# Kernel optimization log

Measured on AMD Instinct MI355X. Metric: run time of the kernel, lower is better.

Reference implementation:

```python
import jax, jax.numpy as jnp
import numpy as np

B, L, NV = 16, 512, 321
D, PL, ST = 128, 16, 8
P = (L - PL) // ST + 2  # 64 patches (replication pad of `stride` on the right)
E, K, H = 8, 2, 512     # experts, top-n gates, expert hidden (4*d_model)
PRED = 96
BAL_COEF, Z_COEF = 0.01, 0.001


def sinusoidal_pe(n, d):
    pos = np.arange(n)[:, None].astype(np.float32)
    div = np.exp(np.arange(0, d, 2).astype(np.float32) * -(np.log(10000.0) / d))
    pe = np.zeros((n, d), dtype=np.float32)
    pe[:, 0::2] = np.sin(pos * div)
    pe[:, 1::2] = np.cos(pos * div)
    return jnp.asarray(pe)


def setup_inputs() -> dict:
    key = jax.random.key(0)
    ks = jax.random.split(key, 12)
    s = lambda i, shape, sc: jax.random.normal(ks[i], shape, jnp.float32) * sc
    return {
        "x_enc": jax.random.normal(ks[0], (B, L, NV), jnp.float32),
        "x_mark_enc": jax.random.normal(ks[1], (B, L, 4), jnp.float32),
        "x_dec": jax.random.normal(ks[2], (B, PRED, NV), jnp.float32),
        "x_mark_dec": jax.random.normal(ks[3], (B, PRED, 4), jnp.float32),
        "W_val": s(4, (PL, D), PL ** -0.5),
        "W_g": s(5, (D, E), D ** -0.5),
        "W1": s(6, (E, D, H), D ** -0.5),
        "b1": jnp.zeros((E, H), jnp.float32),
        "W2": s(7, (E, H, D), H ** -0.5),
        "b2": jnp.zeros((E, D), jnp.float32),
        "W_head": s(8, (D * P, PRED), (D * P) ** -0.5),
        "b_head": jnp.zeros((PRED,), jnp.float32),
    }


def _forward(x_enc, W_val, W_g, W1, b1, W2, b2, W_head, b_head):
    # RevIN-style instance norm (means detached as in torch .detach())
    means = jax.lax.stop_gradient(jnp.mean(x_enc, axis=1, keepdims=True))
    xc = x_enc - means
    stdev = jnp.sqrt(jnp.var(xc, axis=1, keepdims=True) + 1e-5)
    xn = xc / stdev

    # Patch embedding: [B, NV, L] -> replicate-pad -> unfold -> linear + sinusoidal PE
    x = jnp.transpose(xn, (0, 2, 1))                        # [B, NV, L]
    x = jnp.pad(x, ((0, 0), (0, 0), (0, ST)), mode="edge")  # ReplicationPad1d((0, stride))
    idx = np.arange(P)[:, None] * ST + np.arange(PL)        # [P, PL]
    patches = x[:, :, idx]                                  # [B, NV, P, PL]
    tok = patches.reshape(B * NV, P, PL)
    emb = tok @ W_val + sinusoidal_pe(P, D)[None]           # [N, P, D]

    # MoE: top-n softmax gating (gates not renormalized), balance + router-z aux losses
    t = emb.reshape(-1, D)                                  # [T, D], T = B*NV*P
    logits = t @ W_g                                        # [T, E]
    probs = jax.nn.softmax(logits, axis=-1)
    topv, topi = jax.lax.top_k(probs, K)                    # [T, K]

    out = jnp.zeros_like(t)
    for e in range(E):  # fixed small expert count; each expert is a GELU MLP
        h = jax.nn.gelu(t @ W1[e] + b1[e], approximate=False) @ W2[e] + b2[e]
        g = jnp.sum(jnp.where(topi == e, topv, 0.0), axis=-1)  # gate for expert e (0 if unrouted)
        out = out + g[:, None] * h

    me = jnp.mean(probs, axis=0)                                            # mean router prob per expert
    ce = jnp.mean(jax.nn.one_hot(topi, E, dtype=probs.dtype).sum(1), 0) / K  # dispatch fraction per expert
    balance_loss = E * jnp.sum(me * ce)
    z_loss = jnp.mean(jax.nn.logsumexp(logits, axis=-1) ** 2)
    aux = BAL_COEF * balance_loss + Z_COEF * z_loss

    # FlattenHead: [B, NV, P, D] -> [B, NV, D, P] -> flatten(-2) -> Linear(nf, pred_len)
    enc = out.reshape(B, NV, P, D).transpose(0, 1, 3, 2)    # [B, NV, D, P]
    dec = enc.reshape(B, NV, D * P) @ W_head + b_head        # [B, NV, PRED]
    dec = jnp.transpose(dec, (0, 2, 1))                      # [B, PRED, NV]

    # de-normalize
    dec = dec * stdev[:, 0][:, None, :] + means[:, 0][:, None, :]
    return dec, aux


def reference(x_enc, x_mark_enc, x_dec, x_mark_dec, W_val, W_g, W1, b1, W2, b2, W_head, b_head):
    return _forward(x_enc, W_val, W_g, W1, b1, W2, b2, W_head, b_head)
```

## Files before the change

### kernel.cpp

```cpp
#include <hip/hip_runtime.h>
#include <hip/hip_bf16.h>

typedef unsigned short u16;
typedef unsigned int   u32;
typedef unsigned long long u64;
typedef __attribute__((ext_vector_type(8))) short bf16x8;
typedef __attribute__((ext_vector_type(4))) float f32x4;
typedef __attribute__((ext_vector_type(16))) float f32x16;

#define MFMA16(a,b,c) __builtin_amdgcn_mfma_f32_16x16x32_bf16(a,b,c,0,0,0)
#define MFMA32(a,b,c) __builtin_amdgcn_mfma_f32_32x32x16_bf16(a,b,c,0,0,0)

#define NV_   321
#define B_    16
#define L_    512
#define D_    128
#define P_    64
#define E_    8
#define H_    512
#define NRW   5136
#define NTOK  328704
#define DP_   8192
#define NBUCK 329728

static __device__ __forceinline__ u16 f2bf(float f){
  __hip_bfloat16 h = __float2bfloat16(f);
  return *reinterpret_cast<u16*>(&h);
}

static __device__ __forceinline__ float gelu_f(float x){
  float x2 = x*x;
  float p  = __builtin_fmaf(-0.1029433f, x2, -2.3022083f);
  float a  = x*p;
  float en = exp2f(a);
  float r  = __builtin_amdgcn_rcpf(1.0f + en);
  return x*r;
}

static __device__ __forceinline__ u32 bfadd2(u32 a, u32 b){
  float lo = __uint_as_float(a<<16)           + __uint_as_float(b<<16);
  float hi = __uint_as_float(a&0xffff0000u)   + __uint_as_float(b&0xffff0000u);
  return (u32)f2bf(lo) | ((u32)f2bf(hi)<<16);
}

static constexpr size_t alup(size_t x){ return (x + 255) & ~(size_t)255; }
static constexpr size_t OFF_MEAN = 0;
static constexpr size_t OFF_RSTD = OFF_MEAN + alup((size_t)NRW*4);
static constexpr size_t OFF_STD  = OFF_RSTD + alup((size_t)NRW*4);
static constexpr size_t OFF_XT   = OFF_STD  + alup((size_t)NRW*4);
static constexpr size_t OFF_PE   = OFF_XT   + alup((size_t)NRW*L_*4);
static constexpr size_t OFF_W1T  = OFF_PE   + alup((size_t)P_*D_*4);
static constexpr size_t OFF_W2T  = OFF_W1T  + alup((size_t)E_*H_*D_*2);
static constexpr size_t OFF_WHT  = OFF_W2T  + alup((size_t)E_*D_*H_*2);
static constexpr size_t OFF_T    = OFF_WHT  + alup((size_t)96*DP_*2);
static constexpr size_t OFF_TOPI = OFF_T    + alup((size_t)NTOK*D_*2);
static constexpr size_t OFF_GATE = OFF_TOPI + alup((size_t)NTOK*4);
static constexpr size_t OFF_CNTR = OFF_GATE + alup((size_t)NTOK*8);
static constexpr size_t OFF_BTOK = OFF_CNTR + alup((size_t)1024);
static constexpr size_t OFF_BGT  = OFF_BTOK + alup((size_t)2*NBUCK*4);
static constexpr size_t OFF_OUT  = OFF_BGT  + alup((size_t)2*NBUCK*4);
static constexpr size_t OFF_MEAND= OFF_OUT  + alup((size_t)NTOK*D_*2);
static constexpr size_t OFF_RSTDD= OFF_MEAND+ alup((size_t)NRW*8);
static constexpr size_t OFF_WVG  = OFF_RSTDD+ alup((size_t)NRW*8);
static constexpr size_t OFF_PEG  = OFF_WVG  + alup((size_t)16*8*8);
static constexpr size_t OFF_PG   = OFF_PEG  + alup((size_t)P_*E_*8);
static constexpr size_t OFF_PI   = OFF_PG   + alup((size_t)NRW*12*4);



__global__ void k_xt(const float* __restrict__ x, float* __restrict__ xT){
  __shared__ float tile[32][33];
  int b = blockIdx.z;
  int v0 = blockIdx.x*32, l0 = blockIdx.y*32;
  int tx = threadIdx.x, ty = threadIdx.y;
  for(int i=ty;i<32;i+=8){
    int l = l0+i, v = v0+tx;
    tile[i][tx] = (v<NV_) ? x[((size_t)b*L_ + l)*NV_ + v] : 0.f;
  }
  __syncthreads();
  for(int i=ty;i<32;i+=8){
    int v = v0+i, l = l0+tx;
    if(v<NV_) xT[((size_t)(b*NV_+v))*L_ + l] = tile[tx][i];
  }
}

__global__ void k_stats(const float* __restrict__ xT, float* meanp, float* rstdp, float* stdp,
                        double* meand, double* rstdd){
  __shared__ double s1[256], s2[256];
  int r = blockIdx.x, t = threadIdx.x;
  double a = (double)xT[(size_t)r*L_ + t], b = (double)xT[(size_t)r*L_ + 256 + t];
  s1[t]=a+b; s2[t]=a*a+b*b;
  __syncthreads();
  for(int o=128;o>0;o>>=1){ if(t<o){ s1[t]+=s1[t+o]; s2[t]+=s2[t+o]; } __syncthreads(); }
  if(t==0){
    double m = s1[0]*(1.0/512.0);
    double var = s2[0]*(1.0/512.0) - m*m;
    double sd = sqrt(var + 1e-5);
    meanp[r]=(float)m; stdp[r]=(float)sd; rstdp[r]=(float)(1.0/sd);
    meand[r]=m; rstdd[r]=1.0/sd;
  }
}

__global__ void k_prep(const float* __restrict__ Wval, const float* __restrict__ Wg,
                       float* __restrict__ pef, double* __restrict__ Wvg,
                       double* __restrict__ peg){
  int t = threadIdx.x;
  for(int i=t;i<8192;i+=256){
    int p = i>>7, d = i&127, k = d>>1;
    double div = exp(-(double)(2*k) * (9.210340371976184 /128.0));
    double ang = (double)p * div;
    double v = (d&1) ? cos(ang) : sin(ang);
    pef[i] = (float)v;
  }
  __syncthreads();
  if(t<128){
    int j = t>>3, e = t&7;
    double acc = 0.0;
    for(int d=0;d<128;d++) acc += (double)Wval[j*128+d] * (double)Wg[d*8+e];
    Wvg[t] = acc;
  }
  for(int q=t;q<512;q+=256){
    int p = q>>3, e = q&7;
    double acc = 0.0;
    for(int d=0;d<128;d++) acc += (double)pef[p*128+d] * (double)Wg[d*8+e];
    peg[q] = acc;
  }
}

__global__ void k_wt(const float* __restrict__ in, u16* __restrict__ outp, int R, int C){
  __shared__ float tile[32][33];
  int e = blockIdx.z;
  int c0 = blockIdx.x*32, r0 = blockIdx.y*32;
  const float* src = in + (size_t)e*R*C;
  u16* dst = outp + (size_t)e*R*C;
  int tx=threadIdx.x, ty=threadIdx.y;
  for(int i=ty;i<32;i+=8){
    int r=r0+i, c=c0+tx;
    tile[i][tx] = (r<R && c<C) ? src[(size_t)r*C+c] : 0.f;
  }
  __syncthreads();
  for(int i=ty;i<32;i+=8){
    int c=c0+i, r=r0+tx;
    if(c<C && r<R) dst[(size_t)c*R + r] = f2bf(tile[tx][i]);
  }
}

__global__ void k_wh(const float* __restrict__ Wh, u16* __restrict__ WhT2){
  __shared__ float tile[32][33];
  int d0 = blockIdx.x*32, o0 = blockIdx.y*32, p = blockIdx.z;
  int tx = threadIdx.x, ty = threadIdx.y;
  for(int i=ty;i<32;i+=8){
    int r = (d0+i)*64 + p;
    tile[i][tx] = Wh[(size_t)r*96 + o0 + tx];
  }
  __syncthreads();
  for(int i=ty;i<32;i+=8){
    int o = o0+i;
    WhT2[(size_t)o*DP_ + p*128 + d0 + tx] = f2bf(tile[tx][i]);
  }
}

__global__ __launch_bounds__(256) void k_embed(
    const float* __restrict__ xT, const float* __restrict__ meanp, const float* __restrict__ rstdp,
    const float* __restrict__ Wval, const float* __restrict__ pe,
    u16* __restrict__ tglob)
{
  __shared__ __align__(16) float xn[520];
  int r = blockIdx.x, t = threadIdx.x;
  float mean = meanp[r], rstd = rstdp[r];
  float v0 = (xT[(size_t)r*L_ + t]       - mean)*rstd;
  float v1 = (xT[(size_t)r*L_ + 256 + t] - mean)*rstd;
  xn[t] = v0; xn[t+256] = v1;
  if(t==255){
    #pragma unroll
    for(int i=512;i<520;i++) xn[i]=v1;
  }
  int d0 = (t & 63)*2;
  int p0 = t >> 6;
  float2 w[16];
  #pragma unroll
  for(int j=0;j<16;j++) w[j] = *(const float2*)(Wval + j*128 + d0);
  __syncthreads();

  for(int p=p0;p<64;p+=4){
    const float4* xp = (const float4*)(xn + p*8);
    float4 x0=xp[0], x1=xp[1], x2=xp[2], x3=xp[3];
    float xv[16];
    *(float4*)(xv+0)=x0; *(float4*)(xv+4)=x1; *(float4*)(xv+8)=x2; *(float4*)(xv+12)=x3;
    float2 pw = *(const float2*)(pe + p*128 + d0);
    float a0 = pw.x, a1 = pw.y;
    #pragma unroll
    for(int j=0;j<16;j++){ a0 += xv[j]*w[j].x; a1 += xv[j]*w[j].y; }
    u32 packed = (u32)f2bf(a0) | ((u32)f2bf(a1)<<16);
    *(u32*)(tglob + ((size_t)(r*64+p)*128 + d0)) = packed;
  }
}

__global__ __launch_bounds__(256) void k_gate(
    const float* __restrict__ xT, const double* __restrict__ meand, const double* __restrict__ rstdd,
    const double* __restrict__ Wvg, const double* __restrict__ peg,
    int* __restrict__ topip, float2* __restrict__ gatep,
    float* __restrict__ pg, int* __restrict__ pib)
{
  __shared__ double xn[520];
  __shared__ double lgt[64][9];
  int r = blockIdx.x, t = threadIdx.x;
  double m = meand[r], rs = rstdd[r];
  double v0 = ((double)xT[(size_t)r*L_ + t]       - m)*rs;
  double v1 = ((double)xT[(size_t)r*L_ + 256 + t] - m)*rs;
  xn[t]=v0; xn[t+256]=v1;
  if(t==255){
    #pragma unroll
    for(int i=512;i<520;i++) xn[i]=v1;
  }
  __syncthreads();
  for(int q=t;q<512;q+=256){
    int p = q>>3, e = q&7;
    double acc = peg[q];
    #pragma unroll
    for(int j=0;j<16;j++) acc += xn[p*8+j]*Wvg[j*8+e];
    lgt[p][e] = acc;
  }
  __syncthreads();
  if(t<64){
    int token = r*64 + t;
    double l0[8];
    #pragma unroll
    for(int e=0;e<8;e++) l0[e]=lgt[t][e];
    double mx=l0[0];
    #pragma unroll
    for(int e=1;e<8;e++) mx = fmax(mx,l0[e]);
    int i1=0; double b1v=l0[0];
    #pragma unroll
    for(int e=1;e<8;e++) if(l0[e]>b1v){b1v=l0[e]; i1=e;}
    int i2=-1; double b2v=-1e300;
    #pragma unroll
    for(int e=0;e<8;e++) if(e!=i1 && l0[e]>b2v){b2v=l0[e]; i2=e;}
    float pr[8]; float sum=0.f;
    #pragma unroll
    for(int e=0;e<8;e++){ pr[e]=__expf((float)(l0[e]-mx)); sum+=pr[e]; }
    float inv = 1.f/sum;
    #pragma unroll
    for(int e=0;e<8;e++) pr[e]*=inv;
    topip[token] = i1 | (i2<<8);
    gatep[token] = make_float2(pr[i1], pr[i2]);
    float lse = (float)mx + __logf(sum);
    #pragma unroll
    for(int e=0;e<8;e++){
      float v = pr[e];
      for(int o=32;o>0;o>>=1) v += __shfl_down(v,o);
      if(t==0) pg[r*12+e] = v;
    }
    {
      float z = lse*lse;
      for(int o=32;o>0;o>>=1) z += __shfl_down(z,o);
      if(t==0) pg[r*12+8] = z;
    }
    #pragma unroll
    for(int e=0;e<8;e++){
      u64 m1 = __ballot(i1==e);
      u64 m2 = __ballot(i2==e);
      if(t==0){
        pib[r*16+e]   = (int)__popcll(m1);
        pib[r*16+8+e] = (int)__popcll(m2);
      }
    }
  }
}

__global__ __launch_bounds__(256) void k_aux(const float* __restrict__ pg, const int* __restrict__ pib,
                                             int* __restrict__ ci, float* __restrict__ dout){
  __shared__ double sd[256];
  __shared__ int si[256];
  __shared__ double totd[9];
  __shared__ int toti[16];
  int t = threadIdx.x;
  double accd[9]; int acci[16];
  #pragma unroll
  for(int c=0;c<9;c++) accd[c]=0.0;
  #pragma unroll
  for(int c=0;c<16;c++) acci[c]=0;
  for(int r=t;r<NRW;r+=256){
    #pragma unroll
    for(int c=0;c<9;c++) accd[c] += (double)pg[r*12+c];
    #pragma unroll
    for(int c=0;c<16;c++) acci[c] += pib[r*16+c];
  }
  for(int c=0;c<9;c++){
    sd[t]=accd[c]; __syncthreads();
    for(int o=128;o>0;o>>=1){ if(t<o) sd[t]+=sd[t+o]; __syncthreads(); }
    if(t==0) totd[c]=sd[0];
    __syncthreads();
  }
  for(int c=0;c<16;c++){
    si[t]=acci[c]; __syncthreads();
    for(int o=128;o>0;o>>=1){ if(t<o) si[t]+=si[t+o]; __syncthreads(); }
    if(t==0) toti[c]=si[0];
    __syncthreads();
  }
  if(t==0){
    const double invN = 1.0/(double)NTOK;
    double bal = 0.0;
    int es1=0, bs1=0, es2=0, bs2=0;
    for(int e=0;e<8;e++){
      int c1 = toti[e], c2 = toti[8+e];
      bal += (totd[e]*invN) * ((double)(c1+c2) * invN * 0.5);
      ci[32+e]=es1; ci[16+e]=es1; ci[50+e]=bs1;
      ci[41+e]=es2; ci[24+e]=es2; ci[59+e]=bs2;
      es1 += c1; bs1 += (c1+127)>>7;
      es2 += c2; bs2 += (c2+127)>>7;
    }
    ci[40]=es1; ci[58]=bs1;
    ci[49]=es2; ci[67]=bs2;
    dout[493056] = (float)(0.01*8.0*bal + 0.001*(totd[8]*invN));
  }
}

__global__ __launch_bounds__(256) void k_scatter(const int* __restrict__ topip,
    const float2* __restrict__ gatep, int* __restrict__ ci,
    int* __restrict__ btok, float* __restrict__ bgt){
  __shared__ int lc[16]; __shared__ int lb[16];
  int t = threadIdx.x;
  int token = blockIdx.x*256 + t;
  if(t<16) lc[t]=0;
  __syncthreads();
  int ti = topip[token];
  float2 g = gatep[token];
  int e1 = ti & 255, e2 = (ti>>8)&255;
  int r1 = atomicAdd(&lc[e1],1);
  int r2 = atomicAdd(&lc[8+e2],1);
  __syncthreads();
  if(t<8)            lb[t] = atomicAdd(&ci[16+t],   lc[t]);
  else if(t<16)      lb[t] = atomicAdd(&ci[24+t-8], lc[t]);
  __syncthreads();
  int p1 = lb[e1]+r1, p2 = lb[8+e2]+r2;
  btok[p1] = token;         bgt[p1] = g.x;
  btok[NBUCK+p2] = token;   bgt[NBUCK+p2] = g.y;
}

__global__ __launch_bounds__(256,3) void k_expert(
    const u16* __restrict__ tglob,
    const u16* __restrict__ W1T, const u16* __restrict__ W2T,
    const float* __restrict__ b1g, const float* __restrict__ b2g,
    const int* __restrict__ ci,
    const int* __restrict__ btok, const float* __restrict__ bgt,
    u16* __restrict__ outg, int slot)
{
  __shared__ __align__(16) u16 Wb[2][9472];
  __shared__ __align__(16) u16 Ss[128*40];
  __shared__ float gtA[128];
  __shared__ int   tkA[128];

  int bid = blockIdx.x, t = threadIdx.x;
  int stB = 32 + slot*9, bsB = 50 + slot*9;
  int boff = slot*NBUCK;
  if(bid >= ci[bsB+8]) return;
  int e = 0;
  #pragma unroll
  for(int k2=1;k2<8;k2++) if(bid >= ci[bsB+k2]) e = k2;
  int row0 = ci[stB+e] + (bid - ci[bsB+e])*128;
  int rend = ci[stB+e+1];

  if(t<128){
    int pos = row0+t;
    bool v = pos<rend;
    gtA[t] = v ? bgt[boff+pos]  : 0.f;
    tkA[t] = v ? btok[boff+pos] : -1;
  }

  int wid = t>>6, lane = t&63;
  int m = lane&31, hi = lane>>5;
  int rb = wid*32;

  int posA = row0 + rb + m;
  int tokA = (posA<rend) ? btok[boff+posA] : 0;
  const u16* arow = tglob + (size_t)tokA*128 + hi*8;
  bf16x8 areg[8];
  #pragma unroll
  for(int ks=0;ks<8;ks++) areg[ks] = *(const bf16x8*)(arow + ks*16);

  int hr = t>>3, q = t&7;
  int dr = t>>1, q2 = t&1;

  {
    const u16* s1 = W1T + ((size_t)e*H_ + hr)*128 + q*16;
    u16* d1 = &Wb[0][hr*136 + q*16];
    *(uint4*)(d1)   = *(const uint4*)(s1);
    *(uint4*)(d1+8) = *(const uint4*)(s1+8);
    const u16* s2 = W2T + ((size_t)e*D_ + dr)*H_ + q2*16;
    u16* d2 = &Wb[0][4352 + dr*40 + q2*16];
    *(uint4*)(d2)   = *(const uint4*)(s2);
    *(uint4*)(d2+8) = *(const uint4*)(s2+8);
  }
  __syncthreads();

  f32x16 accO[4];
  const f32x16 z16 = {0,0,0,0,0,0,0,0,0,0,0,0,0,0,0,0};
  #pragma unroll
  for(int nt=0;nt<4;nt++) accO[nt] = z16;

  for(int hc=0;hc<16;hc++){
    const u16* W1c = &Wb[hc&1][0];
    const u16* W2c = &Wb[hc&1][4352];
    uint4 l0,l1,l2,l3;
    if(hc<15){
      const u16* s1 = W1T + ((size_t)e*H_ + (hc+1)*32 + hr)*128 + q*16;
      l0 = *(const uint4*)(s1); l1 = *(const uint4*)(s1+8);
      const u16* s2 = W2T + ((size_t)e*D_ + dr)*H_ + (hc+1)*32 + q2*16;
      l2 = *(const uint4*)(s2); l3 = *(const uint4*)(s2+8);
    }
    f32x16 acc1 = z16;
    #pragma unroll
    for(int ks=0;ks<8;ks++){
      bf16x8 b = *(const bf16x8*)(W1c + m*136 + ks*16 + hi*8);
      acc1 = MFMA32(areg[ks], b, acc1);
    }
    float bv = b1g[e*H_ + hc*32 + m];
    #pragma unroll
    for(int reg=0; reg<16; reg++){
      int rl = (reg&3) + 8*(reg>>2) + 4*hi;
      Ss[(rb+rl)*40 + m] = f2bf(gelu_f(acc1[reg] + bv));
    }
    #pragma unroll
    for(int ks=0;ks<2;ks++){
      bf16x8 a = *(const bf16x8*)(Ss + (rb+m)*40 + ks*16 + hi*8);
      #pragma unroll
      for(int nt=0;nt<4;nt++){
        bf16x8 b = *(const bf16x8*)(W2c + (nt*32+m)*40 + ks*16 + hi*8);
        accO[nt] = MFMA32(a, b, accO[nt]);
      }
    }
    if(hc<15){
      u16* d1 = &Wb[(hc+1)&1][hr*136 + q*16];
      *(uint4*)(d1)   = l0; *(uint4*)(d1+8) = l1;
      u16* d2 = &Wb[(hc+1)&1][4352 + dr*40 + q2*16];
      *(uint4*)(d2)   = l2; *(uint4*)(d2+8) = l3;
      __syncthreads();
    }
  }

  float b2v[4];
  #pragma unroll
  for(int nt=0;nt<4;nt++) b2v[nt] = b2g[e*128 + nt*32 + m];
  float gts[16];
  #pragma unroll
  for(int reg=0; reg<16; reg++){
    int rl = (reg&3) + 8*(reg>>2) + 4*hi;
    gts[reg] = gtA[rb+rl];
  }
  int lr2 = lane>>1, hf = lane&1;
  int tok2 = tkA[rb+lr2];
  u16* dstbase = outg + (size_t)((tok2<0)?0:tok2)*128 + hf*16;
  #pragma unroll
  for(int nt=0;nt<4;nt++){
    #pragma unroll
    for(int reg=0; reg<16; reg++){
      int rl = (reg&3) + 8*(reg>>2) + 4*hi;
      Ss[(rb+rl)*40 + m] = f2bf((accO[nt][reg] + b2v[nt]) * gts[reg]);
    }
    __builtin_amdgcn_s_waitcnt(0);
    if(tok2>=0){
      const u16* sp = Ss + (rb+lr2)*40 + hf*16;
      uint4 v0 = *(const uint4*)(sp);
      uint4 v1 = *(const uint4*)(sp+8);
      u16* dp = dstbase + nt*32;
      if(slot==1){
        uint4 o0 = *(const uint4*)(dp), o1 = *(const uint4*)(dp+8);
        v0.x=bfadd2(v0.x,o0.x); v0.y=bfadd2(v0.y,o0.y);
        v0.z=bfadd2(v0.z,o0.z); v0.w=bfadd2(v0.w,o0.w);
        v1.x=bfadd2(v1.x,o1.x); v1.y=bfadd2(v1.y,o1.y);
        v1.z=bfadd2(v1.z,o1.z); v1.w=bfadd2(v1.w,o1.w);
      }
      *(uint4*)(dp)   = v0;
      *(uint4*)(dp+8) = v1;
    }
    __builtin_amdgcn_s_waitcnt(0);
  }
}

__global__ __launch_bounds__(256) void k_head(const u16* __restrict__ Aout,
    const u16* __restrict__ WhT2, float* __restrict__ dec8){
  int bid = blockIdx.x;
  int mb = bid>>3, kseg = bid&7;
  int t = threadIdx.x, wid = t>>6, lane = t&63;
  int quad = lane>>4, li = lane&15;
  int r0 = mb*64 + wid*16;
  int rowA = r0 + li; if(rowA >= NRW) rowA = NRW-1;
  const u16* aptr = Aout + (size_t)rowA*DP_ + kseg*1024 + quad*8;
  const u16* bptr = WhT2 + (size_t)li*DP_  + kseg*1024 + quad*8;
  f32x4 acc[6];
  #pragma unroll
  for(int j=0;j<6;j++) acc[j]=(f32x4){0,0,0,0};
  #pragma unroll 4
  for(int ks=0;ks<32;ks++){
    bf16x8 af = *(const bf16x8*)(aptr + ks*32);
    #pragma unroll
    for(int nt=0;nt<6;nt++){
      bf16x8 bw = *(const bf16x8*)(bptr + (size_t)nt*16*DP_ + ks*32);
      acc[nt] = MFMA16(af, bw, acc[nt]);
    }
  }
  float* dst = dec8 + (size_t)kseg*NRW*96;
  #pragma unroll
  for(int nt=0;nt<6;nt++)
    #pragma unroll
    for(int rg=0;rg<4;rg++){
      int mm = r0 + quad*4 + rg;
      if(mm < NRW) dst[(size_t)mm*96 + nt*16 + li] = acc[nt][rg];
    }
}

__global__ void k_final(const float* __restrict__ dec8, const float* __restrict__ bhead,
    const float* __restrict__ stdp, const float* __restrict__ meanp, float* __restrict__ outp){
  __shared__ float s[64*97];
  int b = blockIdx.y, v0 = blockIdx.x*64;
  int t = threadIdx.x;
  for(int i=t;i<6144;i+=256){
    int vi = i/96, o = i - vi*96;
    int v = v0+vi;
    float acc = 0.f;
    if(v<NV_){
      size_t base = (size_t)(b*NV_+v)*96 + o;
      #pragma unroll
      for(int ks=0;ks<8;ks++) acc += dec8[(size_t)ks*NRW*96 + base];
    }
    s[vi*97+o] = acc;
  }
  __syncthreads();
  for(int i=t;i<6144;i+=256){
    int o = i>>6, vi = i&63;
    int v = v0+vi;
    if(v<NV_){
      int r = b*NV_+v;
      outp[((size_t)b*96 + o)*NV_ + v] = (s[vi*97+o] + bhead[o])*stdp[r] + meanp[r];
    }
  }
}

extern "C" void kernel_launch(void* const* d_in, const int* in_sizes, int n_in,
                              void* d_out, int out_size, void* d_ws, size_t ws_size,
                              hipStream_t stream){
  const float* x_enc = (const float*)d_in[0];
  const float* W_val = (const float*)d_in[4];
  const float* W_g   = (const float*)d_in[5];
  const float* W1    = (const float*)d_in[6];
  const float* b1    = (const float*)d_in[7];
  const float* W2    = (const float*)d_in[8];
  const float* b2    = (const float*)d_in[9];
  const float* W_head= (const float*)d_in[10];
  const float* b_head= (const float*)d_in[11];
  float* outp = (float*)d_out;
  char* ws = (char*)d_ws;

  float* meanp = (float*)(ws+OFF_MEAN);
  float* rstdp = (float*)(ws+OFF_RSTD);
  float* stdp  = (float*)(ws+OFF_STD);
  float* xT    = (float*)(ws+OFF_XT);
  float* pe    = (float*)(ws+OFF_PE);
  u16*   W1T   = (u16*)(ws+OFF_W1T);
  u16*   W2T   = (u16*)(ws+OFF_W2T);
  u16*   WhT2  = (u16*)(ws+OFF_WHT);
  u16*   tglob = (u16*)(ws+OFF_T);
  float* dec8  = (float*)(ws+OFF_T);
  int*   topip = (int*)(ws+OFF_TOPI);
  float2* gatep= (float2*)(ws+OFF_GATE);
  int*   ci    = (int*)(ws+OFF_CNTR+128);
  int*   btok  = (int*)(ws+OFF_BTOK);
  float* bgt   = (float*)(ws+OFF_BGT);
  u16*   outg  = (u16*)(ws+OFF_OUT);
  double* meand= (double*)(ws+OFF_MEAND);
  double* rstdd= (double*)(ws+OFF_RSTDD);
  double* Wvg  = (double*)(ws+OFF_WVG);
  double* peg  = (double*)(ws+OFF_PEG);
  float* pg    = (float*)(ws+OFF_PG);
  int*   pib   = (int*)(ws+OFF_PI);

  hipMemsetAsync(ws+OFF_CNTR, 0, 1024, stream);

  k_xt<<<dim3(11,16,B_), dim3(32,8), 0, stream>>>(x_enc, xT);
  k_stats<<<NRW, 256, 0, stream>>>(xT, meanp, rstdp, stdp, meand, rstdd);
  k_prep<<<1, 256, 0, stream>>>(W_val, W_g, pe, Wvg, peg);
  k_wt<<<dim3(16,4,E_), dim3(32,8), 0, stream>>>(W1, W1T, 128, 512);
  k_wt<<<dim3(4,16,E_), dim3(32,8), 0, stream>>>(W2, W2T, 512, 128);
  k_wh<<<dim3(4,3,64), dim3(32,8), 0, stream>>>(W_head, WhT2);
  k_embed<<<NRW, 256, 0, stream>>>(xT, meanp, rstdp, W_val, pe, tglob);
  k_gate<<<NRW, 256, 0, stream>>>(xT, meand, rstdd, Wvg, peg, topip, gatep, pg, pib);
  k_aux<<<1, 256, 0, stream>>>(pg, pib, ci, outp);
  k_scatter<<<NTOK/256, 256, 0, stream>>>(topip, gatep, ci, btok, bgt);
  k_expert<<<2576, 256, 0, stream>>>(tglob, W1T, W2T, b1, b2, ci, btok, bgt, outg, 0);
  k_expert<<<2576, 256, 0, stream>>>(tglob, W1T, W2T, b1, b2, ci, btok, bgt, outg, 1);
  k_head<<<648, 256, 0, stream>>>(outg, WhT2, dec8);
  k_final<<<dim3(6,B_), 256, 0, stream>>>(dec8, b_head, stdp, meanp, outp);
}
```

Baseline: 652.0 us.

## Fuse embed and gate kernels; transpose expert second GEMM for direct row stores

Merges the patch-embedding and gating kernels into one launch, so xT is read once and the per-row normalization is shared. In the expert kernel the second MFMA swaps its operands so each lane holds one token's output columns. Gate, bias and accumulate are then applied in registers and written straight to global memory, dropping the shared-memory staging and waitcnt barriers of the old epilogue. GELU is computed in pairs, and the stores become narrower 8-byte writes, which may coalesce less well.

```diff
diff --git a/kernel.cpp b/kernel.cpp
--- a/kernel.cpp
+++ b/kernel.cpp
@@ -5,6 +5,7 @@
 typedef unsigned int   u32;
 typedef unsigned long long u64;
 typedef __attribute__((ext_vector_type(8))) short bf16x8;
+typedef __attribute__((ext_vector_type(2))) float f32x2;
 typedef __attribute__((ext_vector_type(4))) float f32x4;
 typedef __attribute__((ext_vector_type(16))) float f32x16;
 
@@ -28,12 +29,16 @@
   return *reinterpret_cast<u16*>(&h);
 }
 
-static __device__ __forceinline__ float gelu_f(float x){
-  float x2 = x*x;
-  float p  = __builtin_fmaf(-0.1029433f, x2, -2.3022083f);
-  float a  = x*p;
-  float en = exp2f(a);
-  float r  = __builtin_amdgcn_rcpf(1.0f + en);
+static __device__ __forceinline__ f32x2 gelu2(f32x2 x){
+  f32x2 x2 = x*x;
+  f32x2 p  = x2 * (-0.1029433f) + (-2.3022083f);
+  f32x2 a  = x*p;
+  f32x2 en;
+  en.x = exp2f(a.x); en.y = exp2f(a.y);
+  f32x2 den = en + 1.0f;
+  f32x2 r;
+  r.x = __builtin_amdgcn_rcpf(den.x);
+  r.y = __builtin_amdgcn_rcpf(den.y);
   return x*r;
 }
 
@@ -160,20 +165,30 @@
   }
 }
 
-__global__ __launch_bounds__(256) void k_embed(
+__global__ __launch_bounds__(256) void k_embgate(
     const float* __restrict__ xT, const float* __restrict__ meanp, const float* __restrict__ rstdp,
+    const double* __restrict__ meand, const double* __restrict__ rstdd,
     const float* __restrict__ Wval, const float* __restrict__ pe,
-    u16* __restrict__ tglob)
+    const double* __restrict__ Wvg, const double* __restrict__ peg,
+    u16* __restrict__ tglob, int* __restrict__ topip, float2* __restrict__ gatep,
+    float* __restrict__ pg, int* __restrict__ pib)
 {
   __shared__ __align__(16) float xn[520];
+  __shared__ double xnd[520];
+  __shared__ double lgt[64][9];
   int r = blockIdx.x, t = threadIdx.x;
   float mean = meanp[r], rstd = rstdp[r];
-  float v0 = (xT[(size_t)r*L_ + t]       - mean)*rstd;
-  float v1 = (xT[(size_t)r*L_ + 256 + t] - mean)*rstd;
+  double md = meand[r], rsd = rstdd[r];
+  float x0f = xT[(size_t)r*L_ + t], x1f = xT[(size_t)r*L_ + 256 + t];
+  float v0 = (x0f - mean)*rstd;
+  float v1 = (x1f - mean)*rstd;
+  double d0v = ((double)x0f - md)*rsd;
+  double d1v = ((double)x1f - md)*rsd;
   xn[t] = v0; xn[t+256] = v1;
+  xnd[t] = d0v; xnd[t+256] = d1v;
   if(t==255){
     #pragma unroll
-    for(int i=512;i<520;i++) xn[i]=v1;
+    for(int i=512;i<520;i++){ xn[i]=v1; xnd[i]=d1v; }
   }
   int d0 = (t & 63)*2;
   int p0 = t >> 6;
@@ -184,9 +199,9 @@
 
   for(int p=p0;p<64;p+=4){
     const float4* xp = (const float4*)(xn + p*8);
-    float4 x0=xp[0], x1=xp[1], x2=xp[2], x3=xp[3];
+    float4 a0_=xp[0], a1_=xp[1], a2_=xp[2], a3_=xp[3];
     float xv[16];
-    *(float4*)(xv+0)=x0; *(float4*)(xv+4)=x1; *(float4*)(xv+8)=x2; *(float4*)(xv+12)=x3;
+    *(float4*)(xv+0)=a0_; *(float4*)(xv+4)=a1_; *(float4*)(xv+8)=a2_; *(float4*)(xv+12)=a3_;
     float2 pw = *(const float2*)(pe + p*128 + d0);
     float a0 = pw.x, a1 = pw.y;
     #pragma unroll
@@ -194,31 +209,12 @@
     u32 packed = (u32)f2bf(a0) | ((u32)f2bf(a1)<<16);
     *(u32*)(tglob + ((size_t)(r*64+p)*128 + d0)) = packed;
   }
-}
-
-__global__ __launch_bounds__(256) void k_gate(
-    const float* __restrict__ xT, const double* __restrict__ meand, const double* __restrict__ rstdd,
-    const double* __restrict__ Wvg, const double* __restrict__ peg,
-    int* __restrict__ topip, float2* __restrict__ gatep,
-    float* __restrict__ pg, int* __restrict__ pib)
-{
-  __shared__ double xn[520];
-  __shared__ double lgt[64][9];
-  int r = blockIdx.x, t = threadIdx.x;
-  double m = meand[r], rs = rstdd[r];
-  double v0 = ((double)xT[(size_t)r*L_ + t]       - m)*rs;
-  double v1 = ((double)xT[(size_t)r*L_ + 256 + t] - m)*rs;
-  xn[t]=v0; xn[t+256]=v1;
-  if(t==255){
-    #pragma unroll
-    for(int i=512;i<520;i++) xn[i]=v1;
-  }
-  __syncthreads();
+
   for(int q=t;q<512;q+=256){
     int p = q>>3, e = q&7;
     double acc = peg[q];
     #pragma unroll
-    for(int j=0;j<16;j++) acc += xn[p*8+j]*Wvg[j*8+e];
+    for(int j=0;j<16;j++) acc += xnd[p*8+j]*Wvg[j*8+e];
     lgt[p][e] = acc;
   }
   __syncthreads();
@@ -348,8 +344,7 @@
 {
   __shared__ __align__(16) u16 Wb[2][9472];
   __shared__ __align__(16) u16 Ss[128*40];
-  __shared__ float gtA[128];
-  __shared__ int   tkA[128];
+  __shared__ float b2s[128];
 
   int bid = blockIdx.x, t = threadIdx.x;
   int stB = 32 + slot*9, bsB = 50 + slot*9;
@@ -361,19 +356,16 @@
   int row0 = ci[stB+e] + (bid - ci[bsB+e])*128;
   int rend = ci[stB+e+1];
 
-  if(t<128){
-    int pos = row0+t;
-    bool v = pos<rend;
-    gtA[t] = v ? bgt[boff+pos]  : 0.f;
-    tkA[t] = v ? btok[boff+pos] : -1;
-  }
+  if(t<128) b2s[t] = b2g[e*128+t];
 
   int wid = t>>6, lane = t&63;
   int m = lane&31, hi = lane>>5;
   int rb = wid*32;
 
   int posA = row0 + rb + m;
-  int tokA = (posA<rend) ? btok[boff+posA] : 0;
+  bool valid = posA < rend;
+  int tokA = valid ? btok[boff+posA] : 0;
+  float gt  = valid ? bgt[boff+posA] : 0.f;
   const u16* arow = tglob + (size_t)tokA*128 + hi*8;
   bf16x8 areg[8];
   #pragma unroll
@@ -417,17 +409,22 @@
     }
     float bv = b1g[e*H_ + hc*32 + m];
     #pragma unroll
-    for(int reg=0; reg<16; reg++){
+    for(int pr=0; pr<8; pr++){
+      int reg = pr*2;
       int rl = (reg&3) + 8*(reg>>2) + 4*hi;
-      Ss[(rb+rl)*40 + m] = f2bf(gelu_f(acc1[reg] + bv));
+      f32x2 v; v.x = acc1[reg]+bv; v.y = acc1[reg+1]+bv;
+      f32x2 g2 = gelu2(v);
+      u16* sp = Ss + (rb+rl)*40 + m;
+      sp[0]  = f2bf(g2.x);
+      sp[40] = f2bf(g2.y);
     }
     #pragma unroll
     for(int ks=0;ks<2;ks++){
-      bf16x8 a = *(const bf16x8*)(Ss + (rb+m)*40 + ks*16 + hi*8);
+      bf16x8 sfrag = *(const bf16x8*)(Ss + (rb+m)*40 + ks*16 + hi*8);
       #pragma unroll
-      for(int nt=0;nt<4;nt++){
-        bf16x8 b = *(const bf16x8*)(W2c + (nt*32+m)*40 + ks*16 + hi*8);
-        accO[nt] = MFMA32(a, b, accO[nt]);
+      for(int mt=0;mt<4;mt++){
+        bf16x8 wfrag = *(const bf16x8*)(W2c + (mt*32+m)*40 + ks*16 + hi*8);
+        accO[mt] = MFMA32(wfrag, sfrag, accO[mt]);
       }
     }
     if(hc<15){
@@ -439,42 +436,29 @@
     }
   }
 
-  float b2v[4];
-  #pragma unroll
-  for(int nt=0;nt<4;nt++) b2v[nt] = b2g[e*128 + nt*32 + m];
-  float gts[16];
-  #pragma unroll
-  for(int reg=0; reg<16; reg++){
-    int rl = (reg&3) + 8*(reg>>2) + 4*hi;
-    gts[reg] = gtA[rb+rl];
-  }
-  int lr2 = lane>>1, hf = lane&1;
-  int tok2 = tkA[rb+lr2];
-  u16* dstbase = outg + (size_t)((tok2<0)?0:tok2)*128 + hf*16;
-  #pragma unroll
-  for(int nt=0;nt<4;nt++){
-    #pragma unroll
-    for(int reg=0; reg<16; reg++){
-      int rl = (reg&3) + 8*(reg>>2) + 4*hi;
-      Ss[(rb+rl)*40 + m] = f2bf((accO[nt][reg] + b2v[nt]) * gts[reg]);
-    }
-    __builtin_amdgcn_s_waitcnt(0);
-    if(tok2>=0){
-      const u16* sp = Ss + (rb+lr2)*40 + hf*16;
-      uint4 v0 = *(const uint4*)(sp);
-      uint4 v1 = *(const uint4*)(sp+8);
-      u16* dp = dstbase + nt*32;
-      if(slot==1){
-        uint4 o0 = *(const uint4*)(dp), o1 = *(const uint4*)(dp+8);
-        v0.x=bfadd2(v0.x,o0.x); v0.y=bfadd2(v0.y,o0.y);
-        v0.z=bfadd2(v0.z,o0.z); v0.w=bfadd2(v0.w,o0.w);
-        v1.x=bfadd2(v1.x,o1.x); v1.y=bfadd2(v1.y,o1.y);
-        v1.z=bfadd2(v1.z,o1.z); v1.w=bfadd2(v1.w,o1.w);
+  u16* dst = outg + (size_t)tokA*128;
+  #pragma unroll
+  for(int mt=0;mt<4;mt++){
+    #pragma unroll
+    for(int rg=0;rg<4;rg++){
+      int dd = mt*32 + rg*8 + hi*4;
+      float4 bb = *(const float4*)(b2s + dd);
+      float f0 = (accO[mt][rg*4+0] + bb.x)*gt;
+      float f1 = (accO[mt][rg*4+1] + bb.y)*gt;
+      float f2 = (accO[mt][rg*4+2] + bb.z)*gt;
+      float f3 = (accO[mt][rg*4+3] + bb.w)*gt;
+      u32 w0 = (u32)f2bf(f0) | ((u32)f2bf(f1)<<16);
+      u32 w1 = (u32)f2bf(f2) | ((u32)f2bf(f3)<<16);
+      if(valid){
+        u32* dp = (u32*)(dst + dd);
+        if(slot==1){
+          w0 = bfadd2(w0, dp[0]);
+          w1 = bfadd2(w1, dp[1]);
+        }
+        uint2 wv; wv.x = w0; wv.y = w1;
+        *(uint2*)dp = wv;
       }
-      *(uint4*)(dp)   = v0;
-      *(uint4*)(dp+8) = v1;
-    }
-    __builtin_amdgcn_s_waitcnt(0);
+    }
   }
 }
 
@@ -583,8 +567,8 @@
   k_wt<<<dim3(16,4,E_), dim3(32,8), 0, stream>>>(W1, W1T, 128, 512);
   k_wt<<<dim3(4,16,E_), dim3(32,8), 0, stream>>>(W2, W2T, 512, 128);
   k_wh<<<dim3(4,3,64), dim3(32,8), 0, stream>>>(W_head, WhT2);
-  k_embed<<<NRW, 256, 0, stream>>>(xT, meanp, rstdp, W_val, pe, tglob);
-  k_gate<<<NRW, 256, 0, stream>>>(xT, meand, rstdd, Wvg, peg, topip, gatep, pg, pib);
+  k_embgate<<<NRW, 256, 0, stream>>>(xT, meanp, rstdp, meand, rstdd, W_val, pe,
+                                     Wvg, peg, tglob, topip, gatep, pg, pib);
   k_aux<<<1, 256, 0, stream>>>(pg, pib, ci, outp);
   k_scatter<<<NTOK/256, 256, 0, stream>>>(topip, gatep, ci, btok, bgt);
   k_expert<<<2576, 256, 0, stream>>>(tglob, W1T, W2T, b1, b2, ci, btok, bgt, outg, 0);
```

After: 661.2 us. No clear change (+1.4%).
